# Optimization experiments

Hardware: AMD Instinct MI355X
Metric: run time of the kernel (lower is better)

Reference implementation:

```python
import jax, jax.numpy as jnp
import numpy as np

EPS = 1e-12


def _l2norm(x, axis):
    return x / jnp.maximum(jnp.linalg.norm(x, axis=axis, keepdims=True), EPS)


def _wn_weight(v, g):
    # weight norm over input axis (kernel_size=1): W = g * v / ||v||
    return g * v / jnp.maximum(jnp.linalg.norm(v, axis=0, keepdims=True), EPS)


def setup_inputs() -> dict:
    key = jax.random.key(0)
    ks = jax.random.split(key, 8)
    B, T, D = 16, 4096, 512
    N, K, d = 9, 1024, 8
    return {
        "z": jax.random.normal(ks[0], (B, T, D), dtype=jnp.float32),
        "in_v": jax.random.normal(ks[1], (N, D, d), dtype=jnp.float32) * 0.05,
        "in_g": jax.random.uniform(ks[2], (N, d), dtype=jnp.float32) + 0.5,
        "in_b": jax.random.normal(ks[3], (N, d), dtype=jnp.float32) * 0.01,
        "out_v": jax.random.normal(ks[4], (N, d, D), dtype=jnp.float32) * 0.05,
        "out_g": jax.random.uniform(ks[5], (N, D), dtype=jnp.float32) + 0.5,
        "out_b": jax.random.normal(ks[6], (N, D), dtype=jnp.float32) * 0.01,
        "codebooks": jax.random.normal(ks[7], (N, K, d), dtype=jnp.float32),
    }


def reference(z, in_v, in_g, in_b, out_v, out_g, out_b, codebooks):
    # Eval-mode ResidualVectorQuantize: n_quantizers = n_codebooks, mask all True.
    n_codebooks = codebooks.shape[0]
    residual = z
    z_q = jnp.zeros_like(z)
    commitment_loss = jnp.zeros((), z.dtype)
    codebook_loss = jnp.zeros((), z.dtype)
    codes, latents = [], []
    for i in range(n_codebooks):
        # in_proj (weight-normalized 1x1 conv == linear): [B,T,D] -> [B,T,d]
        W_in = _wn_weight(in_v[i], in_g[i])
        z_e = jnp.einsum("btd,dc->btc", residual, W_in) + in_b[i]
        # decode_latents: l2-normalize, pairwise sq-dist, nearest neighbor
        cb = codebooks[i]                      # [K, d] raw codebook
        enc_n = _l2norm(z_e, axis=-1)          # [B, T, d]
        cb_n = _l2norm(cb, axis=-1)            # [K, d]
        dist = (jnp.sum(enc_n * enc_n, -1, keepdims=True)
                - 2.0 * jnp.einsum("btc,kc->btk", enc_n, cb_n)
                + jnp.sum(cb_n * cb_n, -1))    # [B, T, K]
        indices = jnp.argmax(-dist, axis=-1)   # [B, T]
        z_q_i = cb[indices]                    # gather from raw codebook [B,T,d]
        # per-batch losses (mean over T, d)
        commit_i = jnp.mean((z_e - jax.lax.stop_gradient(z_q_i)) ** 2, axis=(1, 2))
        cbloss_i = jnp.mean((z_q_i - jax.lax.stop_gradient(z_e)) ** 2, axis=(1, 2))
        # straight-through estimator
        z_q_st = z_e + jax.lax.stop_gradient(z_q_i - z_e)
        # out_proj: [B,T,d] -> [B,T,D]
        W_out = _wn_weight(out_v[i], out_g[i])
        z_q_proj = jnp.einsum("btc,cd->btd", z_q_st, W_out) + out_b[i]
        z_q = z_q + z_q_proj
        residual = residual - z_q_proj
        commitment_loss = commitment_loss + commit_i.mean()
        codebook_loss = codebook_loss + cbloss_i.mean()
        codes.append(indices)
        latents.append(z_e)
    codes = jnp.stack(codes, axis=2)           # [B, T, N]
    latents = jnp.concatenate(latents, axis=2) # [B, T, N*d]
    return z_q, codes, latents, commitment_loss, codebook_loss
```

## Files before the change

### kernel.cpp

```cpp
#include <hip/hip_runtime.h>
#include <math.h>

#define ROWS   65536

#define WS_WPAD 0
#define WS_WOUT 49152
#define WS_CBT  86016
#define WS_SC   159744
#define WS_M    168960
#define WS_CACC 174144
#define WS_SOB  174216
#define WS_LOSS 174728

#define OUT_CODES 33554432
#define OUT_LAT   34144256
#define OUT_CLOSS 38862848
#define OUT_CBLOSS 38862849

__device__ __forceinline__ int pcol(int cc){ return (cc/9)*12 + (cc%9); }

__global__ __launch_bounds__(256) void prep1(const float* __restrict__ in_v,
    const float* __restrict__ in_g, const float* __restrict__ out_v,
    const float* __restrict__ out_g, const float* __restrict__ out_b,
    const float* __restrict__ cb, float* __restrict__ ws)
{
    int t = blockIdx.x*256 + threadIdx.x;
    if (t < 9216) {
        int i = t >> 10, k = t & 1023;
        const float* p = cb + (i*1024 + k)*8;
        float v[8]; float ssq = 0.f;
        #pragma unroll
        for (int c=0;c<8;c++){ v[c]=p[c]; ssq = fmaf(v[c],v[c],ssq); }
        float den = fmaxf(sqrtf(ssq), 1e-12f);
        float sc = 0.f;
        #pragma unroll
        for (int c=0;c<8;c++){ float cn = v[c]/den; ws[WS_CBT + (i*8+c)*1024 + k] = cn; sc = fmaf(cn,cn,sc); }
        ws[WS_SC + i*1024 + k] = sc;
    } else if (t < 13824) {
        int r = t - 9216; int j = r >> 9, tt = r & 511;
        float v[8]; float ssq = 0.f;
        #pragma unroll
        for (int a=0;a<8;a++){ v[a]=out_v[(j*8+a)*512+tt]; ssq=fmaf(v[a],v[a],ssq); }
        float den = fmaxf(sqrtf(ssq), 1e-12f);
        float g = out_g[j*512+tt];
        #pragma unroll
        for (int a=0;a<8;a++) ws[WS_WOUT + (j*8+a)*512 + tt] = g*v[a]/den;
    } else if (t < 18432) {
        int r = t - 13824;
        int w = r >> 6, l = r & 63;
        int i = w >> 3, c = w & 7;
        float v[8]; float ssq = 0.f;
        #pragma unroll
        for (int u=0;u<8;u++){ v[u] = in_v[(i*512 + l*8+u)*8 + c]; ssq = fmaf(v[u],v[u],ssq); }
        #pragma unroll
        for (int off=1; off<64; off<<=1) ssq += __shfl_xor(ssq, off, 64);
        float den = fmaxf(sqrtf(ssq), 1e-12f);
        float g = in_g[i*8+c];
        int pc = pcol(i*8+c);
        #pragma unroll
        for (int u=0;u<8;u++) ws[WS_WPAD + (l*8+u)*96 + pc] = g*v[u]/den;
    } else if (t < 18944) {
        int tt = t - 18432;
        float s = 0.f;
        for (int j=0;j<9;j++) s += out_b[j*512+tt];
        ws[WS_SOB + tt] = s;
    } else if (t == 18944) {
        *(double*)&ws[WS_LOSS] = 0.0;
    }
}

__global__ __launch_bounds__(256) void prep2(const float* __restrict__ out_b,
                                             float* __restrict__ ws)
{
    int g = blockIdx.x*256 + threadIdx.x;
    if (g < 41472) {
        int oi = g >> 3, part = g & 7;
        int j = oi / 576; int rem = oi % 576; int i = rem >> 6; int ab = rem & 63;
        int a = ab >> 3, b = ab & 7;
        int pc = pcol(i*8+b);
        const float* wo = ws + WS_WOUT + (j*8+a)*512 + part*64;
        const float* wp = ws + WS_WPAD + (part*64)*96 + pc;
        float s = 0.f;
        #pragma unroll
        for (int u=0; u<16; u++) {
            float4 w4 = *(const float4*)(wo + u*4);
            s = fmaf(w4.x, wp[(u*4+0)*96], s);
            s = fmaf(w4.y, wp[(u*4+1)*96], s);
            s = fmaf(w4.z, wp[(u*4+2)*96], s);
            s = fmaf(w4.w, wp[(u*4+3)*96], s);
        }
        #pragma unroll
        for (int off=1; off<8; off<<=1) s += __shfl_xor(s, off, 64);
        if (part == 0) ws[WS_M + oi] = s;
    } else if (g < 42048) {
        int r = g - 41472;
        int oi = r >> 3, part = r & 7;
        int i = oi >> 3, b = oi & 7;
        int pc = pcol(i*8+b);
        float s = 0.f;
        for (int u=0; u<64; u++) {
            int tt = part*64 + u;
            float bb = 0.f;
            for (int j=0;j<i;j++) bb += out_b[j*512+tt];
            s = fmaf(bb, ws[WS_WPAD + tt*96+pc], s);
        }
        #pragma unroll
        for (int off=1; off<8; off<<=1) s += __shfl_xor(s, off, 64);
        if (part == 0) ws[WS_CACC + oi] = s;
    }
}

__global__ __launch_bounds__(256) void gemm_in(const float* __restrict__ z,
    const float* __restrict__ in_b, const float* __restrict__ ws, float* __restrict__ out)
{
    __shared__ float AsT[32*132];
    __shared__ float Bs[32*96];
    int tid = threadIdx.x;
    int rowbase = blockIdx.x * 128;
    int tr = tid & 31, tc = tid >> 5;
    float acc[4][9];
    #pragma unroll
    for (int r=0;r<4;r++){
        #pragma unroll
        for(int c=0;c<9;c++) acc[r][c]=0.f;
    }
    int kq = tid & 7, rr = tid >> 3;
    for (int kk=0; kk<16; kk++) {
        #pragma unroll
        for (int p=0;p<4;p++){
            int row = rr + p*32;
            float4 a = *(const float4*)(z + (size_t)(rowbase+row)*512 + kk*32 + kq*4);
            AsT[(kq*4+0)*132 + row] = a.x;
            AsT[(kq*4+1)*132 + row] = a.y;
            AsT[(kq*4+2)*132 + row] = a.z;
            AsT[(kq*4+3)*132 + row] = a.w;
        }
        #pragma unroll
        for (int p=0;p<3;p++){
            int idx = p*256 + tid;
            *(float4*)(Bs + idx*4) = *(const float4*)(ws + WS_WPAD + kk*32*96 + idx*4);
        }
        __syncthreads();
        #pragma unroll 4
        for (int k=0;k<32;k++){
            float4 a  = *(const float4*)(AsT + k*132 + tr*4);
            float4 b0 = *(const float4*)(Bs + k*96 + tc*12);
            float4 b1 = *(const float4*)(Bs + k*96 + tc*12 + 4);
            float  b8 = Bs[k*96 + tc*12 + 8];
            float av[4] = {a.x,a.y,a.z,a.w};
            float bv[9] = {b0.x,b0.y,b0.z,b0.w,b1.x,b1.y,b1.z,b1.w,b8};
            #pragma unroll
            for (int r=0;r<4;r++){
                #pragma unroll
                for (int c=0;c<9;c++) acc[r][c] = fmaf(av[r], bv[c], acc[r][c]);
            }
        }
        __syncthreads();
    }
    #pragma unroll
    for (int c=0;c<9;c++){
        int cc = tc*9+c;
        float bias = in_b[cc];
        #pragma unroll
        for (int r=0;r<4;r++){
            int row = rowbase + tr*4 + r;
            out[OUT_LAT + (size_t)row*72 + cc] = acc[r][c] + bias;
        }
    }
}

__global__ __launch_bounds__(256) void step_kernel(int i,
    const float* __restrict__ cbooks, float* __restrict__ ws, float* __restrict__ out)
{
    __shared__ float lds_cb[8*1040];
    __shared__ float lds_sc[4*260];
    __shared__ float warr[4];
    int tid = threadIdx.x;
    #pragma unroll
    for (int p=0;p<8;p++){
        int s = (p*256 + tid)*4;
        int c = s >> 10; int r = s & 1023; int qq = r >> 8; int kk = r & 255;
        float4 v = *(const float4*)(ws + WS_CBT + i*8192 + s);
        *(float4*)(lds_cb + c*1040 + qq*260 + kk) = v;
    }
    {
        int s = tid*4;
        int qq = s >> 8; int kk = s & 255;
        float4 v = *(const float4*)(ws + WS_SC + i*1024 + s);
        *(float4*)(lds_sc + qq*260 + kk) = v;
    }
    __syncthreads();

    int gid = blockIdx.x*256 + tid;
    int row = gid >> 2;
    int q = tid & 3;

    float* lat = out + OUT_LAT + (size_t)row*72 + i*8;
    float4 p0 = *(const float4*)(lat);
    float4 p1 = *(const float4*)(lat+4);
    float ze[8] = {p0.x,p0.y,p0.z,p0.w,p1.x,p1.y,p1.z,p1.w};
    #pragma unroll
    for (int b=0;b<8;b++) ze[b] -= ws[WS_CACC + i*8 + b];
    for (int j=0;j<i;j++){
        int kj = (int)out[OUT_CODES + (size_t)row*9 + j];
        const float* qp = cbooks + (j*1024+kj)*8;
        float4 q0 = *(const float4*)(qp);
        float4 q1 = *(const float4*)(qp+4);
        float qa[8] = {q0.x,q0.y,q0.z,q0.w,q1.x,q1.y,q1.z,q1.w};
        const float* M = ws + WS_M + (j*9+i)*64;
        #pragma unroll
        for (int a=0;a<8;a++){
            #pragma unroll
            for (int b=0;b<8;b++) ze[b] = fmaf(-qa[a], M[a*8+b], ze[b]);
        }
    }
    float ssq = 0.f;
    #pragma unroll
    for (int c=0;c<8;c++) ssq = fmaf(ze[c],ze[c],ssq);
    float den = fmaxf(sqrtf(ssq), 1e-12f);
    float zen[8];
    #pragma unroll
    for (int c=0;c<8;c++) zen[c] = ze[c]/den;
    float se = 0.f;
    #pragma unroll
    for (int c=0;c<8;c++) se = fmaf(zen[c],zen[c],se);

    const float* cbq = lds_cb + q*260;
    const float* scq = lds_sc + q*260;
    float bestd = 1e30f; int bestk = 0;
    const int kbase = q*256;
    #pragma unroll 2
    for (int kk=0; kk<256; kk+=4){
        float d0=0.f,d1=0.f,d2=0.f,d3=0.f;
        #pragma unroll
        for (int c=0;c<8;c++){
            float4 v = *(const float4*)(cbq + c*1040 + kk);
            d0 = fmaf(zen[c], v.x, d0);
            d1 = fmaf(zen[c], v.y, d1);
            d2 = fmaf(zen[c], v.z, d2);
            d3 = fmaf(zen[c], v.w, d3);
        }
        float4 sc4 = *(const float4*)(scq + kk);
        float t0 = fmaf(d0,-2.0f,se)+sc4.x;
        float t1 = fmaf(d1,-2.0f,se)+sc4.y;
        float t2 = fmaf(d2,-2.0f,se)+sc4.z;
        float t3 = fmaf(d3,-2.0f,se)+sc4.w;
        bool c0 = t0<bestd; bestk = c0?(kbase+kk+0):bestk; bestd = c0?t0:bestd;
        bool c1 = t1<bestd; bestk = c1?(kbase+kk+1):bestk; bestd = c1?t1:bestd;
        bool c2 = t2<bestd; bestk = c2?(kbase+kk+2):bestk; bestd = c2?t2:bestd;
        bool c3 = t3<bestd; bestk = c3?(kbase+kk+3):bestk; bestd = c3?t3:bestd;
    }
    #pragma unroll
    for (int off=1; off<4; off<<=1){
        float od = __shfl_xor(bestd, off, 64);
        int   ok = __shfl_xor(bestk, off, 64);
        if (od < bestd || (od == bestd && ok < bestk)) { bestd = od; bestk = ok; }
    }

    float lpart = 0.f;
    if (q == 0){
        out[OUT_CODES + (size_t)row*9 + i] = (float)bestk;
        float4 z0 = {ze[0],ze[1],ze[2],ze[3]};
        float4 z1 = {ze[4],ze[5],ze[6],ze[7]};
        *(float4*)(lat)   = z0;
        *(float4*)(lat+4) = z1;
        const float* qp = cbooks + (i*1024+bestk)*8;
        #pragma unroll
        for (int c=0;c<8;c++){ float dd = ze[c]-qp[c]; lpart = fmaf(dd,dd,lpart); }
    }
    #pragma unroll
    for (int off=1; off<64; off<<=1) lpart += __shfl_xor(lpart, off, 64);
    if ((tid & 63)==0) warr[tid>>6] = lpart;
    __syncthreads();
    if (tid==0){
        double bs = (double)warr[0]+(double)warr[1]+(double)warr[2]+(double)warr[3];
        atomicAdd((double*)&ws[WS_LOSS], bs);
    }
}

__global__ __launch_bounds__(256) void gemm_out(const float* __restrict__ cbooks,
    const float* __restrict__ ws, float* __restrict__ out)
{
    __shared__ float QL[64*76];
    __shared__ float Ws[72*128];
    int tid = threadIdx.x;
    int rowbase = blockIdx.x*64;
    if (tid < 64){
        int row = rowbase + tid;
        for (int j=0;j<9;j++){
            int kj = (int)out[OUT_CODES + (size_t)row*9 + j];
            const float* qp = cbooks + (j*1024+kj)*8;
            float4 q0 = *(const float4*)qp;
            float4 q1 = *(const float4*)(qp+4);
            *(float4*)(QL + tid*76 + j*8)     = q0;
            *(float4*)(QL + tid*76 + j*8 + 4) = q1;
        }
    }
    int tr = tid & 15, tc = tid >> 4;
    for (int cc=0; cc<4; cc++){
        __syncthreads();
        #pragma unroll
        for (int p=0;p<9;p++){
            int idx = p*256 + tid;
            int jr = idx >> 5; int cq = idx & 31;
            *(float4*)(Ws + jr*128 + cq*4) = *(const float4*)(ws + WS_WOUT + jr*512 + cc*128 + cq*4);
        }
        __syncthreads();
        float acc[4][8];
        #pragma unroll
        for (int r=0;r<4;r++){
            #pragma unroll
            for (int c=0;c<8;c++) acc[r][c]=0.f;
        }
        #pragma unroll 4
        for (int k=0;k<72;k++){
            float a0 = QL[(tr*4+0)*76 + k];
            float a1 = QL[(tr*4+1)*76 + k];
            float a2 = QL[(tr*4+2)*76 + k];
            float a3 = QL[(tr*4+3)*76 + k];
            float4 b0 = *(const float4*)(Ws + k*128 + tc*8);
            float4 b1 = *(const float4*)(Ws + k*128 + tc*8 + 4);
            float bv[8] = {b0.x,b0.y,b0.z,b0.w,b1.x,b1.y,b1.z,b1.w};
            float av[4] = {a0,a1,a2,a3};
            #pragma unroll
            for (int r=0;r<4;r++){
                #pragma unroll
                for (int c=0;c<8;c++) acc[r][c] = fmaf(av[r], bv[c], acc[r][c]);
            }
        }
        float4 s0 = *(const float4*)(ws + WS_SOB + cc*128 + tc*8);
        float4 s1 = *(const float4*)(ws + WS_SOB + cc*128 + tc*8 + 4);
        #pragma unroll
        for (int r=0;r<4;r++){
            int row = rowbase + tr*4 + r;
            float4 o0 = {acc[r][0]+s0.x, acc[r][1]+s0.y, acc[r][2]+s0.z, acc[r][3]+s0.w};
            float4 o1 = {acc[r][4]+s1.x, acc[r][5]+s1.y, acc[r][6]+s1.z, acc[r][7]+s1.w};
            *(float4*)(out + (size_t)row*512 + cc*128 + tc*8)     = o0;
            *(float4*)(out + (size_t)row*512 + cc*128 + tc*8 + 4) = o1;
        }
    }
    if (blockIdx.x==0 && tid==0){
        double L = *(const double*)(ws + WS_LOSS);
        float lv = (float)(L * (1.0/524288.0));
        out[OUT_CLOSS]  = lv;
        out[OUT_CBLOSS] = lv;
    }
}

extern "C" void kernel_launch(void* const* d_in, const int* in_sizes, int n_in,
                              void* d_out, int out_size, void* d_ws, size_t ws_size,
                              hipStream_t stream) {
    const float* z     = (const float*)d_in[0];
    const float* in_v  = (const float*)d_in[1];
    const float* in_g  = (const float*)d_in[2];
    const float* in_b  = (const float*)d_in[3];
    const float* out_v = (const float*)d_in[4];
    const float* out_g = (const float*)d_in[5];
    const float* out_b = (const float*)d_in[6];
    const float* cb    = (const float*)d_in[7];
    float* out = (float*)d_out;
    float* ws  = (float*)d_ws;

    prep1<<<75, 256, 0, stream>>>(in_v, in_g, out_v, out_g, out_b, cb, ws);
    prep2<<<165, 256, 0, stream>>>(out_b, ws);
    gemm_in<<<512, 256, 0, stream>>>(z, in_b, ws, out);
    for (int i=0; i<9; i++)
        step_kernel<<<1024, 256, 0, stream>>>(i, cb, ws, out);
    gemm_out<<<1024, 256, 0, stream>>>(cb, ws, out);
}
```

Baseline: 672.7 us.

## Restructure VQ step kernel to share codebook loads across rows; prefetch gemm_in tiles

The codebook search now gives each wave 8 rows, with its 64 lanes striding over codebook entries. Each codebook value read from LDS is therefore reused for 8 rows, instead of 4 threads per row each scanning a quarter of the codebook. The residual correction from earlier codebooks is spread across lane groups and combined with shuffles, and the codebook is stored row-major so it can be loaded as float4 halves. gemm_in also software-prefetches the next k-tile of z and the weights into registers while computing the current tile. In exchange there are more registers per thread, a longer cross-lane argmin reduction over 8 rows, and an extra block barrier.

```diff
diff --git a/kernel.cpp b/kernel.cpp
--- a/kernel.cpp
+++ b/kernel.cpp
@@ -5,7 +5,7 @@
 
 #define WS_WPAD 0
 #define WS_WOUT 49152
-#define WS_CBT  86016
+#define WS_CBN  86016
 #define WS_SC   159744
 #define WS_M    168960
 #define WS_CACC 174144
@@ -33,8 +33,9 @@
         for (int c=0;c<8;c++){ v[c]=p[c]; ssq = fmaf(v[c],v[c],ssq); }
         float den = fmaxf(sqrtf(ssq), 1e-12f);
         float sc = 0.f;
-        #pragma unroll
-        for (int c=0;c<8;c++){ float cn = v[c]/den; ws[WS_CBT + (i*8+c)*1024 + k] = cn; sc = fmaf(cn,cn,sc); }
+        float* dst = ws + WS_CBN + (i*1024+k)*8;
+        #pragma unroll
+        for (int c=0;c<8;c++){ float cn = v[c]/den; dst[c] = cn; sc = fmaf(cn,cn,sc); }
         ws[WS_SC + i*1024 + k] = sc;
     } else if (t < 13824) {
         int r = t - 9216; int j = r >> 9, tt = r & 511;
@@ -125,22 +126,30 @@
         for(int c=0;c<9;c++) acc[r][c]=0.f;
     }
     int kq = tid & 7, rr = tid >> 3;
+    const float* zb = z + (size_t)rowbase*512;
+    float4 az[4], bz[3];
+    #pragma unroll
+    for (int p=0;p<4;p++) az[p] = *(const float4*)(zb + (size_t)(rr+p*32)*512 + kq*4);
+    #pragma unroll
+    for (int p=0;p<3;p++) bz[p] = *(const float4*)(ws + WS_WPAD + (p*256+tid)*4);
     for (int kk=0; kk<16; kk++) {
         #pragma unroll
         for (int p=0;p<4;p++){
             int row = rr + p*32;
-            float4 a = *(const float4*)(z + (size_t)(rowbase+row)*512 + kk*32 + kq*4);
-            AsT[(kq*4+0)*132 + row] = a.x;
-            AsT[(kq*4+1)*132 + row] = a.y;
-            AsT[(kq*4+2)*132 + row] = a.z;
-            AsT[(kq*4+3)*132 + row] = a.w;
-        }
-        #pragma unroll
-        for (int p=0;p<3;p++){
-            int idx = p*256 + tid;
-            *(float4*)(Bs + idx*4) = *(const float4*)(ws + WS_WPAD + kk*32*96 + idx*4);
-        }
+            AsT[(kq*4+0)*132 + row] = az[p].x;
+            AsT[(kq*4+1)*132 + row] = az[p].y;
+            AsT[(kq*4+2)*132 + row] = az[p].z;
+            AsT[(kq*4+3)*132 + row] = az[p].w;
+        }
+        #pragma unroll
+        for (int p=0;p<3;p++) *(float4*)(Bs + (p*256+tid)*4) = bz[p];
         __syncthreads();
+        if (kk < 15){
+            #pragma unroll
+            for (int p=0;p<4;p++) az[p] = *(const float4*)(zb + (size_t)(rr+p*32)*512 + (kk+1)*32 + kq*4);
+            #pragma unroll
+            for (int p=0;p<3;p++) bz[p] = *(const float4*)(ws + WS_WPAD + (kk+1)*32*96 + (p*256+tid)*4);
+        }
         #pragma unroll 4
         for (int k=0;k<32;k++){
             float4 a  = *(const float4*)(AsT + k*132 + tr*4);
@@ -172,107 +181,136 @@
 __global__ __launch_bounds__(256) void step_kernel(int i,
     const float* __restrict__ cbooks, float* __restrict__ ws, float* __restrict__ out)
 {
-    __shared__ float lds_cb[8*1040];
-    __shared__ float lds_sc[4*260];
+    __shared__ float CB0[1024*4];
+    __shared__ float CB1[1024*4];
+    __shared__ float SCs[1024];
+    __shared__ float Ms[512];
+    __shared__ float SCR[4*96];
     __shared__ float warr[4];
     int tid = threadIdx.x;
-    #pragma unroll
-    for (int p=0;p<8;p++){
-        int s = (p*256 + tid)*4;
-        int c = s >> 10; int r = s & 1023; int qq = r >> 8; int kk = r & 255;
-        float4 v = *(const float4*)(ws + WS_CBT + i*8192 + s);
-        *(float4*)(lds_cb + c*1040 + qq*260 + kk) = v;
-    }
-    {
-        int s = tid*4;
-        int qq = s >> 8; int kk = s & 255;
-        float4 v = *(const float4*)(ws + WS_SC + i*1024 + s);
-        *(float4*)(lds_sc + qq*260 + kk) = v;
-    }
+
+    const float* cbn = ws + WS_CBN + i*8192;
+    #pragma unroll
+    for (int u=0; u<4; u++){
+        int c = u*256 + tid;
+        float4 h0 = *(const float4*)(cbn + c*8);
+        float4 h1 = *(const float4*)(cbn + c*8 + 4);
+        *(float4*)(CB0 + c*4) = h0;
+        *(float4*)(CB1 + c*4) = h1;
+    }
+    *(float4*)(SCs + tid*4) = *(const float4*)(ws + WS_SC + i*1024 + tid*4);
+    if (tid < i*64)       Ms[tid]     = ws[WS_M + ((tid>>6)*9 + i)*64 + (tid&63)];
+    if (tid + 256 < i*64) Ms[tid+256] = ws[WS_M + (((tid+256)>>6)*9 + i)*64 + (tid&63)];
+
+    int wave = tid >> 6, L = tid & 63;
+    int r = L & 7, jj = L >> 3;
+    int row = blockIdx.x*32 + wave*8 + r;
     __syncthreads();
 
-    int gid = blockIdx.x*256 + tid;
-    int row = gid >> 2;
-    int q = tid & 3;
-
-    float* lat = out + OUT_LAT + (size_t)row*72 + i*8;
-    float4 p0 = *(const float4*)(lat);
-    float4 p1 = *(const float4*)(lat+4);
-    float ze[8] = {p0.x,p0.y,p0.z,p0.w,p1.x,p1.y,p1.z,p1.w};
-    #pragma unroll
-    for (int b=0;b<8;b++) ze[b] -= ws[WS_CACC + i*8 + b];
-    for (int j=0;j<i;j++){
-        int kj = (int)out[OUT_CODES + (size_t)row*9 + j];
-        const float* qp = cbooks + (j*1024+kj)*8;
-        float4 q0 = *(const float4*)(qp);
-        float4 q1 = *(const float4*)(qp+4);
+    float part[8] = {0,0,0,0,0,0,0,0};
+    if (jj < i) {
+        int kj = (int)out[OUT_CODES + (size_t)row*9 + jj];
+        const float* qp = cbooks + ((size_t)(jj*1024+kj))*8;
+        float4 q0 = *(const float4*)qp, q1 = *(const float4*)(qp+4);
         float qa[8] = {q0.x,q0.y,q0.z,q0.w,q1.x,q1.y,q1.z,q1.w};
-        const float* M = ws + WS_M + (j*9+i)*64;
         #pragma unroll
         for (int a=0;a<8;a++){
-            #pragma unroll
-            for (int b=0;b<8;b++) ze[b] = fmaf(-qa[a], M[a*8+b], ze[b]);
-        }
-    }
-    float ssq = 0.f;
-    #pragma unroll
-    for (int c=0;c<8;c++) ssq = fmaf(ze[c],ze[c],ssq);
-    float den = fmaxf(sqrtf(ssq), 1e-12f);
-    float zen[8];
-    #pragma unroll
-    for (int c=0;c<8;c++) zen[c] = ze[c]/den;
-    float se = 0.f;
-    #pragma unroll
-    for (int c=0;c<8;c++) se = fmaf(zen[c],zen[c],se);
-
-    const float* cbq = lds_cb + q*260;
-    const float* scq = lds_sc + q*260;
-    float bestd = 1e30f; int bestk = 0;
-    const int kbase = q*256;
-    #pragma unroll 2
-    for (int kk=0; kk<256; kk+=4){
-        float d0=0.f,d1=0.f,d2=0.f,d3=0.f;
-        #pragma unroll
-        for (int c=0;c<8;c++){
-            float4 v = *(const float4*)(cbq + c*1040 + kk);
-            d0 = fmaf(zen[c], v.x, d0);
-            d1 = fmaf(zen[c], v.y, d1);
-            d2 = fmaf(zen[c], v.z, d2);
-            d3 = fmaf(zen[c], v.w, d3);
-        }
-        float4 sc4 = *(const float4*)(scq + kk);
-        float t0 = fmaf(d0,-2.0f,se)+sc4.x;
-        float t1 = fmaf(d1,-2.0f,se)+sc4.y;
-        float t2 = fmaf(d2,-2.0f,se)+sc4.z;
-        float t3 = fmaf(d3,-2.0f,se)+sc4.w;
-        bool c0 = t0<bestd; bestk = c0?(kbase+kk+0):bestk; bestd = c0?t0:bestd;
-        bool c1 = t1<bestd; bestk = c1?(kbase+kk+1):bestk; bestd = c1?t1:bestd;
-        bool c2 = t2<bestd; bestk = c2?(kbase+kk+2):bestk; bestd = c2?t2:bestd;
-        bool c3 = t3<bestd; bestk = c3?(kbase+kk+3):bestk; bestd = c3?t3:bestd;
-    }
-    #pragma unroll
-    for (int off=1; off<4; off<<=1){
-        float od = __shfl_xor(bestd, off, 64);
-        int   ok = __shfl_xor(bestk, off, 64);
-        if (od < bestd || (od == bestd && ok < bestk)) { bestd = od; bestk = ok; }
-    }
-
-    float lpart = 0.f;
-    if (q == 0){
-        out[OUT_CODES + (size_t)row*9 + i] = (float)bestk;
+            float4 m0 = *(const float4*)(Ms + jj*64 + a*8);
+            float4 m1 = *(const float4*)(Ms + jj*64 + a*8 + 4);
+            part[0]=fmaf(qa[a],m0.x,part[0]); part[1]=fmaf(qa[a],m0.y,part[1]);
+            part[2]=fmaf(qa[a],m0.z,part[2]); part[3]=fmaf(qa[a],m0.w,part[3]);
+            part[4]=fmaf(qa[a],m1.x,part[4]); part[5]=fmaf(qa[a],m1.y,part[5]);
+            part[6]=fmaf(qa[a],m1.z,part[6]); part[7]=fmaf(qa[a],m1.w,part[7]);
+        }
+    }
+    #pragma unroll
+    for (int off=8; off<64; off<<=1){
+        #pragma unroll
+        for (int b=0;b<8;b++) part[b] += __shfl_xor(part[b], off, 64);
+    }
+
+    float ze[8];
+    if (jj == 0) {
+        float* lat = out + OUT_LAT + (size_t)row*72 + i*8;
+        float4 p0 = *(const float4*)lat, p1 = *(const float4*)(lat+4);
+        float P[8] = {p0.x,p0.y,p0.z,p0.w,p1.x,p1.y,p1.z,p1.w};
+        #pragma unroll
+        for (int b=0;b<8;b++) ze[b] = P[b] - ws[WS_CACC + i*8 + b] - part[b];
         float4 z0 = {ze[0],ze[1],ze[2],ze[3]};
         float4 z1 = {ze[4],ze[5],ze[6],ze[7]};
-        *(float4*)(lat)   = z0;
-        *(float4*)(lat+4) = z1;
-        const float* qp = cbooks + (i*1024+bestk)*8;
+        *(float4*)lat = z0; *(float4*)(lat+4) = z1;
+        float ssq = 0.f;
+        #pragma unroll
+        for (int c=0;c<8;c++) ssq = fmaf(ze[c],ze[c],ssq);
+        float den = fmaxf(sqrtf(ssq), 1e-12f);
+        float zen[8];
+        #pragma unroll
+        for (int c=0;c<8;c++) zen[c] = ze[c]/den;
+        float se = 0.f;
+        #pragma unroll
+        for (int c=0;c<8;c++) se = fmaf(zen[c],zen[c],se);
+        float* s = SCR + wave*96 + r*12;
+        float4 w0 = {zen[0],zen[1],zen[2],zen[3]};
+        float4 w1 = {zen[4],zen[5],zen[6],zen[7]};
+        *(float4*)s = w0; *(float4*)(s+4) = w1; s[8] = se;
+    }
+    __syncthreads();
+
+    float zr[8][8], ser[8];
+    #pragma unroll
+    for (int rr=0; rr<8; rr++){
+        const float* s = SCR + wave*96 + rr*12;
+        float4 a = *(const float4*)s, b = *(const float4*)(s+4);
+        zr[rr][0]=a.x; zr[rr][1]=a.y; zr[rr][2]=a.z; zr[rr][3]=a.w;
+        zr[rr][4]=b.x; zr[rr][5]=b.y; zr[rr][6]=b.z; zr[rr][7]=b.w;
+        ser[rr]=s[8];
+    }
+
+    float bd[8]; int bk[8];
+    #pragma unroll
+    for (int rr=0;rr<8;rr++){ bd[rr]=1e30f; bk[rr]=0; }
+    #pragma unroll 2
+    for (int it=0; it<16; it++){
+        int c = it*64 + L;
+        float4 v0 = *(const float4*)(CB0 + c*4);
+        float4 v1 = *(const float4*)(CB1 + c*4);
+        float scv = SCs[c];
+        #pragma unroll
+        for (int rr=0; rr<8; rr++){
+            float d = 0.f;
+            d = fmaf(zr[rr][0], v0.x, d); d = fmaf(zr[rr][1], v0.y, d);
+            d = fmaf(zr[rr][2], v0.z, d); d = fmaf(zr[rr][3], v0.w, d);
+            d = fmaf(zr[rr][4], v1.x, d); d = fmaf(zr[rr][5], v1.y, d);
+            d = fmaf(zr[rr][6], v1.z, d); d = fmaf(zr[rr][7], v1.w, d);
+            float t = fmaf(d, -2.0f, ser[rr]) + scv;
+            bool cg = t < bd[rr];
+            bk[rr] = cg ? c : bk[rr];
+            bd[rr] = cg ? t : bd[rr];
+        }
+    }
+    #pragma unroll
+    for (int off=1; off<64; off<<=1){
+        #pragma unroll
+        for (int rr=0; rr<8; rr++){
+            float od = __shfl_xor(bd[rr], off, 64);
+            int   ok = __shfl_xor(bk[rr], off, 64);
+            if (od < bd[rr] || (od == bd[rr] && ok < bk[rr])) { bd[rr]=od; bk[rr]=ok; }
+        }
+    }
+
+    float lpart = 0.f;
+    if (L < 8) {
+        int k = bk[L];
+        out[OUT_CODES + (size_t)row*9 + i] = (float)k;
+        const float* qp = cbooks + ((size_t)(i*1024+k))*8;
         #pragma unroll
         for (int c=0;c<8;c++){ float dd = ze[c]-qp[c]; lpart = fmaf(dd,dd,lpart); }
     }
     #pragma unroll
     for (int off=1; off<64; off<<=1) lpart += __shfl_xor(lpart, off, 64);
-    if ((tid & 63)==0) warr[tid>>6] = lpart;
+    if (L == 0) warr[wave] = lpart;
     __syncthreads();
-    if (tid==0){
+    if (tid == 0){
         double bs = (double)warr[0]+(double)warr[1]+(double)warr[2]+(double)warr[3];
         atomicAdd((double*)&ws[WS_LOSS], bs);
     }
@@ -365,6 +403,6 @@
     prep2<<<165, 256, 0, stream>>>(out_b, ws);
     gemm_in<<<512, 256, 0, stream>>>(z, in_b, ws, out);
     for (int i=0; i<9; i++)
-        step_kernel<<<1024, 256, 0, stream>>>(i, cb, ws, out);
+        step_kernel<<<2048, 256, 0, stream>>>(i, cb, ws, out);
     gemm_out<<<1024, 256, 0, stream>>>(cb, ws, out);
 }
```

Result: slower. 825.5 us (+22.7%).
